# Performance work log

Measured on AMD Instinct MI355X. Metric: run time of the kernel, lower is better.

## Reference

```python
import jax, jax.numpy as jnp
import numpy as np

K = 20
EPS = 1e-5
SLOPE = 0.2

def knn(x, k):
    # x: [B, C, N]; returns indices of k nearest neighbors [B, N, k]
    xx = jnp.sum(x * x, axis=1)                      # [B, N]
    inner = jnp.einsum('bcn,bcm->bnm', x, x)         # [B, N, N]
    pd = -xx[:, :, None] + 2.0 * inner - xx[:, None, :]  # negative sq dist
    return jax.lax.top_k(pd, k)[1]

def leaky(y):
    return jnp.where(y > 0, y, SLOPE * y)

def batchnorm(y, g, b, axes):
    mean = jnp.mean(y, axis=axes, keepdims=True)
    var = jnp.var(y, axis=axes, keepdims=True)
    return (y - mean) / jnp.sqrt(var + EPS) * g + b

def edge_conv(x, W, g, b):
    # x: [B, C, N] -> [B, O, N]
    idx = knn(x, K)                                   # [B, N, k]
    xT = jnp.transpose(x, (0, 2, 1))                  # [B, N, C]
    nbr = jax.vmap(lambda xb, ib: xb[ib])(xT, idx)    # [B, N, k, C]
    ctr = jnp.broadcast_to(xT[:, :, None, :], nbr.shape)
    feat = jnp.concatenate([nbr - ctr, ctr], axis=-1) # [B, N, k, 2C]
    y = jnp.einsum('bnkc,oc->bnko', feat, W)          # 1x1 conv
    y = leaky(batchnorm(y, g, b, axes=(0, 1, 2)))
    return jnp.transpose(jnp.max(y, axis=2), (0, 2, 1))  # max over k -> [B, O, N]

def setup_inputs() -> dict:
    key = jax.random.key(0)
    ks = jax.random.split(key, 12)
    B, N = 8, 2048
    c1, c2, c3, c4, emb = 64, 64, 128, 256, 1024
    d = {
        'x':  jax.random.normal(ks[0], (B, 3, N), dtype=jnp.float32),
        'W1': jax.random.normal(ks[1], (c1, 6), dtype=jnp.float32) * 0.2,
        'W2': jax.random.normal(ks[2], (c2, 2 * c1), dtype=jnp.float32) * 0.1,
        'W3': jax.random.normal(ks[3], (c3, 2 * c2), dtype=jnp.float32) * 0.1,
        'W4': jax.random.normal(ks[4], (c4, 2 * c3), dtype=jnp.float32) * 0.08,
        'W5': jax.random.normal(ks[5], (emb, 2 * c4), dtype=jnp.float32) * 0.06,
        'g1': jnp.ones((c1,), jnp.float32), 'b1': jnp.zeros((c1,), jnp.float32),
        'g2': jnp.ones((c2,), jnp.float32), 'b2': jnp.zeros((c2,), jnp.float32),
        'g3': jnp.ones((c3,), jnp.float32), 'b3': jnp.zeros((c3,), jnp.float32),
        'g4': jnp.ones((c4,), jnp.float32), 'b4': jnp.zeros((c4,), jnp.float32),
        'g5': jnp.ones((emb,), jnp.float32), 'b5': jnp.zeros((emb,), jnp.float32),
    }
    return d

def reference(x, W1, W2, W3, W4, W5, g1, b1, g2, b2, g3, b3, g4, b4, g5, b5):
    x1 = edge_conv(x,  W1, g1, b1)   # [B, 64, N]
    x2 = edge_conv(x1, W2, g2, b2)   # [B, 64, N]
    x3 = edge_conv(x2, W3, g3, b3)   # [B, 128, N]
    x4 = edge_conv(x3, W4, g4, b4)   # [B, 256, N]
    cat = jnp.concatenate([x1, x2, x3, x4], axis=1)  # [B, 512, N]
    y = jnp.einsum('bcn,oc->bon', cat, W5)           # [B, 1024, N]
    y = leaky(batchnorm(y, g5[None, :, None], b5[None, :, None], axes=(0, 2)))
    mx = jnp.max(y, axis=2)
    av = jnp.mean(y, axis=2)
    return jnp.concatenate([mx, av], axis=1)         # [B, 2048]
```

## Files before the change

### kernel.cpp

```cpp
#include <hip/hip_runtime.h>
#include <cfloat>

#define BB 8
#define NN 2048
#define KNN 20
#define NCOPY 64
#define EPSV 1e-5f
#define SLOPEV 0.2f

typedef short bf16x8 __attribute__((ext_vector_type(8)));
typedef float f32x4 __attribute__((ext_vector_type(4)));

__device__ __forceinline__ unsigned short f2b(float f) {
    unsigned u = __builtin_bit_cast(unsigned, f);
    unsigned r = (u + 0x7FFFu + ((u >> 16) & 1u)) >> 16;
    return (unsigned short)r;
}
__device__ __forceinline__ short4 f2b4(float4 v) {
    short4 r;
    r.x = (short)f2b(v.x); r.y = (short)f2b(v.y);
    r.z = (short)f2b(v.z); r.w = (short)f2b(v.w);
    return r;
}
__device__ __forceinline__ bf16x8 f2b8(float4 a, float4 b) {
    short4 sa = f2b4(a), sb = f2b4(b);
    bf16x8 r;
    r[0] = sa.x; r[1] = sa.y; r[2] = sa.z; r[3] = sa.w;
    r[4] = sb.x; r[5] = sb.y; r[6] = sb.z; r[7] = sb.w;
    return r;
}


__global__ void transpose0_kernel(const float* __restrict__ x, float* __restrict__ XT0) {
    int e = blockIdx.x * blockDim.x + threadIdx.x;
    if (e >= BB * NN * 3) return;
    int b = e / (NN * 3); int r = e - b * NN * 3; int n = r / 3; int c = r - n * 3;
    XT0[e] = x[((size_t)b * 3 + c) * NN + n];
}

__global__ void wprep_kernel(const float* __restrict__ W, float* __restrict__ WaT,
                             float* __restrict__ WdT, int C, int O) {
    int e = blockIdx.x * blockDim.x + threadIdx.x;
    if (e >= C * O) return;
    int c = e / O, o = e - c * O;
    float a = W[o * 2 * C + c];
    WaT[e] = a;
    WdT[e] = W[o * 2 * C + C + c] - a;
}

__global__ void wprep4b_kernel(const float* __restrict__ W, short* __restrict__ Wab,
                               short* __restrict__ Wdb) {
    int e = blockIdx.x * 256 + threadIdx.x;
    int o = e >> 7, c = e & 127;
    float a = W[o * 256 + c];
    Wab[e] = (short)f2b(a);
    Wdb[e] = (short)f2b(W[o * 256 + 128 + c] - a);
}

__global__ void w5b_kernel(const float* __restrict__ W5, short* __restrict__ W5b) {
    int e = blockIdx.x * 256 + threadIdx.x;
    W5b[e] = (short)f2b(W5[e]);
}


template <int C>
__global__ void xx_kernel(const float* __restrict__ XT, float* __restrict__ xx) {
    int e = blockIdx.x * blockDim.x + threadIdx.x;
    if (e >= BB * NN) return;
    const float* p = &XT[(size_t)e * C];
    float s;
    if constexpr (C % 4 == 0) {
        float s0 = 0, s1 = 0, s2 = 0, s3 = 0;
        for (int c = 0; c < C; c += 4) {
            float4 v = *(const float4*)(p + c);
            s0 += v.x * v.x; s1 += v.y * v.y; s2 += v.z * v.z; s3 += v.w * v.w;
        }
        s = (s0 + s1) + (s2 + s3);
    } else {
        s = p[0] * p[0];
        for (int c = 1; c < C; ++c) s += p[c] * p[c];
    }
    xx[e] = s;
}


template <int C>
__global__ __launch_bounds__(256) void knn_dist_kernel(
    const float* __restrict__ XC,
    const float* __restrict__ XT,
    const float* __restrict__ xx,
    float* __restrict__ pd2,
    int b0) {
    constexpr int BK = 16;
    __shared__ float As[BK][68];
    __shared__ alignas(16) float Bs[BK][64];
    int mt = blockIdx.x, nt = blockIdx.y, bz = blockIdx.z;
    int b = b0 + bz;
    int n0 = nt * 64, m0 = mt * 64;
    int tid = threadIdx.x;
    int tn = tid >> 4, tm = tid & 15;
    float P[4][4][4];
    #pragma unroll
    for (int cl = 0; cl < 4; ++cl)
        #pragma unroll
        for (int i = 0; i < 4; ++i)
            #pragma unroll
            for (int j = 0; j < 4; ++j) P[cl][i][j] = 0.f;

    int arow = tid >> 2, acq = tid & 3;
    int brow = tid >> 4, bmq = tid & 15;
    for (int kb = 0; kb < C / BK; ++kb) {
        if (kb) __syncthreads();
        float4 av = *(const float4*)&XT[((size_t)b * NN + n0 + arow) * C + kb * BK + acq * 4];
        As[acq * 4 + 0][arow] = av.x; As[acq * 4 + 1][arow] = av.y;
        As[acq * 4 + 2][arow] = av.z; As[acq * 4 + 3][arow] = av.w;
        *(float4*)&Bs[brow][bmq * 4] =
            *(const float4*)&XC[((size_t)b * C + kb * BK + brow) * NN + m0 + bmq * 4];
        __syncthreads();
        #pragma unroll
        for (int c = 0; c < BK; ++c) {
            float4 a = *(const float4*)&As[c][tn * 4];
            float4 bv = *(const float4*)&Bs[c][tm * 4];
            int cl = c & 3;
            P[cl][0][0] += a.x * bv.x; P[cl][0][1] += a.x * bv.y; P[cl][0][2] += a.x * bv.z; P[cl][0][3] += a.x * bv.w;
            P[cl][1][0] += a.y * bv.x; P[cl][1][1] += a.y * bv.y; P[cl][1][2] += a.y * bv.z; P[cl][1][3] += a.y * bv.w;
            P[cl][2][0] += a.z * bv.x; P[cl][2][1] += a.z * bv.y; P[cl][2][2] += a.z * bv.z; P[cl][2][3] += a.z * bv.w;
            P[cl][3][0] += a.w * bv.x; P[cl][3][1] += a.w * bv.y; P[cl][3][2] += a.w * bv.z; P[cl][3][3] += a.w * bv.w;
        }
    }
    float4 xm = *(const float4*)&xx[(size_t)b * NN + m0 + tm * 4];
    #pragma unroll
    for (int i = 0; i < 4; ++i) {
        float xrn = xx[(size_t)b * NN + n0 + tn * 4 + i];
        float4 pd;
        float in0 = (P[0][i][0] + P[1][i][0]) + (P[2][i][0] + P[3][i][0]);
        float in1 = (P[0][i][1] + P[1][i][1]) + (P[2][i][1] + P[3][i][1]);
        float in2 = (P[0][i][2] + P[1][i][2]) + (P[2][i][2] + P[3][i][2]);
        float in3 = (P[0][i][3] + P[1][i][3]) + (P[2][i][3] + P[3][i][3]);
        pd.x = (2.0f * in0 - xrn) - xm.x;
        pd.y = (2.0f * in1 - xrn) - xm.y;
        pd.z = (2.0f * in2 - xrn) - xm.z;
        pd.w = (2.0f * in3 - xrn) - xm.w;
        *(float4*)&pd2[((size_t)bz * NN + n0 + tn * 4 + i) * NN + m0 + tm * 4] = pd;
    }
}

#define INS(val, mm) do { \
    float _v = (val); int _m = (mm); \
    bool b1 = _v > v1, b2 = _v > v2, b3 = _v > v3, b4 = _v > v4; \
    i4 = b3 ? i3 : (b4 ? _m : i4);  v4 = b3 ? v3 : (b4 ? _v : v4); \
    i3 = b2 ? i2 : (b3 ? _m : i3);  v3 = b2 ? v2 : (b3 ? _v : v3); \
    i2 = b1 ? i1 : (b2 ? _m : i2);  v2 = b1 ? v1 : (b2 ? _v : v2); \
    i1 = b1 ? _m : i1;              v1 = b1 ? _v : v1; \
} while (0)

__device__ __forceinline__ void sel20_reg(const float4* pv, int lane, int* outp) {
    float v1 = -FLT_MAX, v2 = -FLT_MAX, v3 = -FLT_MAX, v4 = -FLT_MAX;
    int i1 = 0x7FFFFFFF, i2 = 0x7FFFFFFF, i3 = 0x7FFFFFFF, i4 = 0x7FFFFFFF;
    unsigned rm = 0;
    #pragma unroll
    for (int j = 0; j < 8; ++j) {
        int m0 = 4 * lane + 256 * j;
        INS(pv[j].x, m0); INS(pv[j].y, m0 + 1); INS(pv[j].z, m0 + 2); INS(pv[j].w, m0 + 3);
    }
    int depth = 4;
    for (int it = 0; it < KNN; ++it) {
        float bv = v1;
        #pragma unroll
        for (int off = 1; off < 64; off <<= 1) bv = fmaxf(bv, __shfl_xor(bv, off));
        int cand = (v1 == bv) ? i1 : 0x7FFFFFFF;
        int bi = cand;
        #pragma unroll
        for (int off = 1; off < 64; off <<= 1) bi = min(bi, __shfl_xor(bi, off));
        if (lane == 0) outp[it] = bi;
        if (v1 == bv && i1 == bi) {
            rm |= 1u << ((((unsigned)bi >> 6) & 0x1C) | ((unsigned)bi & 3));
            v1 = v2; i1 = i2; v2 = v3; i2 = i3; v3 = v4; i3 = i4;
            v4 = -FLT_MAX; i4 = 0x7FFFFFFF;
            if (--depth == 0) {
                v1 = v2 = v3 = v4 = -FLT_MAX;
                i1 = i2 = i3 = i4 = 0x7FFFFFFF;
                #pragma unroll
                for (int j = 0; j < 8; ++j) {
                    int m0 = 4 * lane + 256 * j;
                    if (!(rm & (1u << (4 * j + 0)))) INS(pv[j].x, m0);
                    if (!(rm & (1u << (4 * j + 1)))) INS(pv[j].y, m0 + 1);
                    if (!(rm & (1u << (4 * j + 2)))) INS(pv[j].z, m0 + 2);
                    if (!(rm & (1u << (4 * j + 3)))) INS(pv[j].w, m0 + 3);
                }
                depth = 4;
            }
        }
    }
}

__global__ __launch_bounds__(256) void knn_sel_kernel(
    const float* __restrict__ pd2, int* __restrict__ idxb, int b0) {
    int tid = threadIdx.x, w = tid >> 6, lane = tid & 63;
    int rg = blockIdx.x * 4 + w;
    int bz = rg >> 11, n = rg & (NN - 1);
    const float* row = pd2 + ((size_t)bz * NN + n) * NN;
    float4 pv[8];
    #pragma unroll
    for (int j = 0; j < 8; ++j) pv[j] = *(const float4*)&row[4 * lane + 256 * j];
    int* outp = idxb + ((size_t)(b0 + bz) * NN + n) * KNN;
    sel20_reg(pv, lane, outp);
}

__global__ __launch_bounds__(256) void knn_c3_kernel(
    const float* __restrict__ XC,
    const float* __restrict__ XT,
    const float* __restrict__ xx, int* __restrict__ idxb) {
    int tid = threadIdx.x, w = tid >> 6, lane = tid & 63;
    int rg = blockIdx.x * 4 + w;
    int b = rg >> 11, n = rg & (NN - 1);
    const float* xt0 = XT + ((size_t)b * NN + n) * 3;
    float s0 = xt0[0], s1 = xt0[1], s2 = xt0[2];
    float xrn = xx[(size_t)b * NN + n];
    float4 pv[8];
    #pragma unroll
    for (int j = 0; j < 8; ++j) {
        int m0 = 4 * lane + 256 * j;
        float4 v0 = *(const float4*)&XC[((size_t)b * 3 + 0) * NN + m0];
        float4 v1 = *(const float4*)&XC[((size_t)b * 3 + 1) * NN + m0];
        float4 v2 = *(const float4*)&XC[((size_t)b * 3 + 2) * NN + m0];
        float4 xm = *(const float4*)&xx[(size_t)b * NN + m0];
        float4 in;
        in.x = v0.x * s0; in.x += v1.x * s1; in.x += v2.x * s2;
        in.y = v0.y * s0; in.y += v1.y * s1; in.y += v2.y * s2;
        in.z = v0.z * s0; in.z += v1.z * s1; in.z += v2.z * s2;
        in.w = v0.w * s0; in.w += v1.w * s1; in.w += v2.w * s2;
        pv[j].x = (2.0f * in.x - xrn) - xm.x;
        pv[j].y = (2.0f * in.y - xrn) - xm.y;
        pv[j].z = (2.0f * in.z - xrn) - xm.z;
        pv[j].w = (2.0f * in.w - xrn) - xm.w;
    }
    int* outp = idxb + ((size_t)b * NN + n) * KNN;
    sel20_reg(pv, lane, outp);
}
#undef INS


template <int C, int O>
__global__ __launch_bounds__(256) void edge_passA_kernel(
    const float* __restrict__ XT, const int* __restrict__ idxb,
    const float* __restrict__ WaT, const float* __restrict__ WdT,
    float* __restrict__ ymaxb, float* __restrict__ yminb, float* __restrict__ stats) {
    constexpr int OT = O / 4;
    constexpr int G = 256 / OT;
    constexpr int KP = (KNN + G - 1) / G;
    constexpr int CP = (C % 4 == 0) ? (C + 4) : C;
    __shared__ alignas(16) float ctr[C];
    __shared__ alignas(16) float nbr[KNN][CP];
    __shared__ alignas(16) float t2[O];
    __shared__ int sidx[KNN];
    __shared__ alignas(16) float red[4][1024];
    int blk = blockIdx.x;
    int b = blk >> 11;
    int tid = threadIdx.x;
    if (tid < KNN) sidx[tid] = idxb[(size_t)blk * KNN + tid];
    for (int e = tid; e < C; e += 256) ctr[e] = XT[(size_t)blk * C + e];
    __syncthreads();
    if constexpr (C % 4 == 0) {
        for (int e = tid; e < KNN * (C / 4); e += 256) {
            int k = e / (C / 4), q = e - k * (C / 4);
            *(float4*)&nbr[k][q * 4] =
                *(const float4*)&XT[((size_t)b * NN + sidx[k]) * C + q * 4];
        }
    } else {
        for (int e = tid; e < KNN * C; e += 256) {
            int k = e / C, c = e - k * C;
            nbr[k][c] = XT[((size_t)b * NN + sidx[k]) * C + c];
        }
    }
    if (tid < O) {
        float s = 0;
        for (int c = 0; c < C; ++c) s += WdT[c * O + tid] * ctr[c];
        t2[tid] = s;
    }
    __syncthreads();
    int og = tid % OT, kg = tid / OT;
    int o0 = og * 4;
    float acc[KP][4];
    #pragma unroll
    for (int j = 0; j < KP; ++j) { acc[j][0] = 0; acc[j][1] = 0; acc[j][2] = 0; acc[j][3] = 0; }
    if constexpr (C % 4 == 0) {
        for (int c = 0; c < C; c += 4) {
            float4 w0 = *(const float4*)&WaT[(c + 0) * O + o0];
            float4 w1 = *(const float4*)&WaT[(c + 1) * O + o0];
            float4 w2 = *(const float4*)&WaT[(c + 2) * O + o0];
            float4 w3 = *(const float4*)&WaT[(c + 3) * O + o0];
            #pragma unroll
            for (int j = 0; j < KP; ++j) {
                int k = kg + j * G;
                if (k < KNN) {
                    float4 nv = *(const float4*)&nbr[k][c];
                    acc[j][0] += nv.x * w0.x + nv.y * w1.x + nv.z * w2.x + nv.w * w3.x;
                    acc[j][1] += nv.x * w0.y + nv.y * w1.y + nv.z * w2.y + nv.w * w3.y;
                    acc[j][2] += nv.x * w0.z + nv.y * w1.z + nv.z * w2.z + nv.w * w3.z;
                    acc[j][3] += nv.x * w0.w + nv.y * w1.w + nv.z * w2.w + nv.w * w3.w;
                }
            }
        }
    } else {
        for (int c = 0; c < C; ++c) {
            float4 w = *(const float4*)&WaT[c * O + o0];
            #pragma unroll
            for (int j = 0; j < KP; ++j) {
                int k = kg + j * G;
                if (k < KNN) {
                    float nv = nbr[k][c];
                    acc[j][0] += nv * w.x; acc[j][1] += nv * w.y;
                    acc[j][2] += nv * w.z; acc[j][3] += nv * w.w;
                }
            }
        }
    }
    float t2a[4];
    *(float4*)t2a = *(const float4*)&t2[o0];
    float vmax[4], vmin[4], vsum[4], vsq[4];
    #pragma unroll
    for (int q = 0; q < 4; ++q) { vmax[q] = -FLT_MAX; vmin[q] = FLT_MAX; vsum[q] = 0; vsq[q] = 0; }
    #pragma unroll
    for (int j = 0; j < KP; ++j) {
        int k = kg + j * G;
        if (k < KNN) {
            #pragma unroll
            for (int q = 0; q < 4; ++q) {
                float y = acc[j][q] + t2a[q];
                vmax[q] = fmaxf(vmax[q], y); vmin[q] = fminf(vmin[q], y);
                vsum[q] += y; vsq[q] += y * y;
            }
        }
    }
    *(float4*)&red[0][kg * O + o0] = make_float4(vmax[0], vmax[1], vmax[2], vmax[3]);
    *(float4*)&red[1][kg * O + o0] = make_float4(vmin[0], vmin[1], vmin[2], vmin[3]);
    *(float4*)&red[2][kg * O + o0] = make_float4(vsum[0], vsum[1], vsum[2], vsum[3]);
    *(float4*)&red[3][kg * O + o0] = make_float4(vsq[0], vsq[1], vsq[2], vsq[3]);
    __syncthreads();
    if (tid < O) {
        float m1 = -FLT_MAX, m2 = FLT_MAX, s1 = 0, s2 = 0;
        #pragma unroll 4
        for (int g = 0; g < G; ++g) {
            m1 = fmaxf(m1, red[0][g * O + tid]);
            m2 = fminf(m2, red[1][g * O + tid]);
            s1 += red[2][g * O + tid];
            s2 += red[3][g * O + tid];
        }
        ymaxb[(size_t)blk * O + tid] = m1;
        yminb[(size_t)blk * O + tid] = m2;
        float* st = &stats[(size_t)(blk & (NCOPY - 1)) * (2 * O)];
        atomicAdd(&st[tid], s1);
        atomicAdd(&st[O + tid], s2);
    }
}


__global__ __launch_bounds__(256) void t2_mfma_kernel(
    const float* __restrict__ XT3, const short* __restrict__ Wdb, float* __restrict__ T2) {
    __shared__ alignas(16) short A[16][136];
    int blk = blockIdx.x;
    int tid = threadIdx.x, w = tid >> 6, lane = tid & 63;
    int n0g = blk * 16;
    for (int ch = tid; ch < 512; ch += 256) {
        int r = ch >> 5, c4 = (ch & 31) << 2;
        float4 v = *(const float4*)&XT3[((size_t)n0g + r) * 128 + c4];
        *(short4*)&A[r][c4] = f2b4(v);
    }
    __syncthreads();
    int arow = lane & 15, aq = lane >> 4;
    bf16x8 af[4];
    #pragma unroll
    for (int ks = 0; ks < 4; ++ks)
        af[ks] = *(const bf16x8*)&A[arow][ks * 32 + aq * 8];
    for (int t = 0; t < 4; ++t) {
        int nt = w * 4 + t;
        f32x4 acc = {0.f, 0.f, 0.f, 0.f};
        const short* bp = Wdb + (size_t)(nt * 16 + arow) * 128 + aq * 8;
        #pragma unroll
        for (int ks = 0; ks < 4; ++ks)
            acc = __builtin_amdgcn_mfma_f32_16x16x32_bf16(af[ks], *(const bf16x8*)(bp + ks * 32), acc, 0, 0, 0);
        #pragma unroll
        for (int r = 0; r < 4; ++r)
            T2[((size_t)n0g + aq * 4 + r) * 256 + nt * 16 + arow] = acc[r];
    }
}


__global__ __launch_bounds__(256) void edge4_mfma_kernel(
    const float* __restrict__ XT, const int* __restrict__ idxb,
    const short* __restrict__ Wab, const float* __restrict__ T2,
    float* __restrict__ ymaxb, float* __restrict__ yminb, float* __restrict__ stats) {
    int blk = blockIdx.x;
    int tid = threadIdx.x, w = tid >> 6, lane = tid & 63;
    int p = blk * 4 + w;
    int b = p >> 11;
    size_t baseC = (size_t)b * NN;
    const int* idxp = idxb + (size_t)p * KNN;
    int arow = lane & 15, aq = lane >> 4;
    int idx0 = idxp[arow];
    int idx1 = (arow < 4) ? idxp[16 + arow] : idx0;
    const float* r0 = &XT[(baseC + idx0) * 128 + aq * 8];
    const float* r1 = &XT[(baseC + idx1) * 128 + aq * 8];
    bf16x8 af0[4], af1[4];
    #pragma unroll
    for (int ks = 0; ks < 4; ++ks) {
        af0[ks] = f2b8(*(const float4*)(r0 + ks * 32), *(const float4*)(r0 + ks * 32 + 4));
        af1[ks] = f2b8(*(const float4*)(r1 + ks * 32), *(const float4*)(r1 + ks * 32 + 4));
    }
    const float* t2p = T2 + (size_t)p * 256;
    float* st = stats + (size_t)(p & (NCOPY - 1)) * 512;
    const short* bp0 = Wab + (size_t)arow * 128 + aq * 8;
    bf16x8 bfc[4];
    #pragma unroll
    for (int ks = 0; ks < 4; ++ks) bfc[ks] = *(const bf16x8*)(bp0 + ks * 32);
    float t2c = t2p[arow];
    for (int nt = 0; nt < 16; ++nt) {
        bf16x8 bfn[4]; float t2n = 0.f;
        if (nt < 15) {
            const short* bpn = Wab + (size_t)((nt + 1) * 16 + arow) * 128 + aq * 8;
            #pragma unroll
            for (int ks = 0; ks < 4; ++ks) bfn[ks] = *(const bf16x8*)(bpn + ks * 32);
            t2n = t2p[(nt + 1) * 16 + arow];
        }
        f32x4 acc0 = {0.f, 0.f, 0.f, 0.f}, acc1 = {0.f, 0.f, 0.f, 0.f};
        #pragma unroll
        for (int ks = 0; ks < 4; ++ks) {
            acc0 = __builtin_amdgcn_mfma_f32_16x16x32_bf16(af0[ks], bfc[ks], acc0, 0, 0, 0);
            acc1 = __builtin_amdgcn_mfma_f32_16x16x32_bf16(af1[ks], bfc[ks], acc1, 0, 0, 0);
        }
        float lmax = -FLT_MAX, lmin = FLT_MAX, ls = 0.f, lsq = 0.f;
        #pragma unroll
        for (int r = 0; r < 4; ++r) {
            float y = acc0[r] + t2c;
            lmax = fmaxf(lmax, y); lmin = fminf(lmin, y); ls += y; lsq += y * y;
        }
        if (aq == 0) {
            #pragma unroll
            for (int r = 0; r < 4; ++r) {
                float y = acc1[r] + t2c;
                lmax = fmaxf(lmax, y); lmin = fminf(lmin, y); ls += y; lsq += y * y;
            }
        }
        #pragma unroll
        for (int off = 16; off < 64; off <<= 1) {
            lmax = fmaxf(lmax, __shfl_xor(lmax, off));
            lmin = fminf(lmin, __shfl_xor(lmin, off));
            ls += __shfl_xor(ls, off);
            lsq += __shfl_xor(lsq, off);
        }
        if (lane < 16) {
            ymaxb[(size_t)p * 256 + nt * 16 + lane] = lmax;
            yminb[(size_t)p * 256 + nt * 16 + lane] = lmin;
            atomicAdd(&st[nt * 16 + lane], ls);
            atomicAdd(&st[256 + nt * 16 + lane], lsq);
        }
        #pragma unroll
        for (int ks = 0; ks < 4; ++ks) bfc[ks] = bfn[ks];
        t2c = t2n;
    }
}


__global__ void finalize_stats_kernel(const float* __restrict__ stats, const float* __restrict__ gg,
                                      const float* __restrict__ bb, float* __restrict__ scsh,
                                      int O, float invM) {
    int o = blockIdx.x * blockDim.x + threadIdx.x;
    if (o >= O) return;
    float s1 = 0, s2 = 0;
    for (int cp = 0; cp < NCOPY; ++cp) {
        s1 += stats[(size_t)cp * 2 * O + o];
        s2 += stats[(size_t)cp * 2 * O + O + o];
    }
    float mean = s1 * invM;
    float var = s2 * invM - mean * mean;
    float scale = gg[o] * rsqrtf(var + EPSV);
    float shift = bb[o] - mean * scale;
    scsh[o] = scale; scsh[O + o] = shift;
}

__global__ void edge_passB_kernel(const float* __restrict__ ymaxb, const float* __restrict__ yminb,
                                  const float* __restrict__ scsh, float* __restrict__ XTout,
                                  float* __restrict__ XCout, int O, int total) {
    int e = blockIdx.x * blockDim.x + threadIdx.x;
    if (e >= total) return;
    int o = e & (O - 1);
    float sc = scsh[o], sh = scsh[O + o];
    float y = (sc >= 0.0f) ? ymaxb[e] : yminb[e];
    float z = sc * y + sh;
    float r = (z > 0.0f) ? z : SLOPEV * z;
    XTout[e] = r;
    if (XCout) {
        int n = (e / O) & (NN - 1);
        int bb_ = e / (O * NN);
        XCout[((size_t)bb_ * O + o) * NN + n] = r;
    }
}


__device__ __forceinline__ void stage_cat_b(short (*A)[520], const float* __restrict__ XT1,
                                            const float* __restrict__ XT2, const float* __restrict__ XT3,
                                            const float* __restrict__ XT4, int n0g, int tid) {
    for (int ch = tid; ch < 32 * 16; ch += 256) { int r = ch >> 4, c4 = (ch & 15) << 2;
        *(short4*)&A[r][c4]       = f2b4(*(const float4*)&XT1[((size_t)n0g + r) * 64 + c4]); }
    for (int ch = tid; ch < 32 * 16; ch += 256) { int r = ch >> 4, c4 = (ch & 15) << 2;
        *(short4*)&A[r][64 + c4]  = f2b4(*(const float4*)&XT2[((size_t)n0g + r) * 64 + c4]); }
    for (int ch = tid; ch < 32 * 32; ch += 256) { int r = ch >> 5, c4 = (ch & 31) << 2;
        *(short4*)&A[r][128 + c4] = f2b4(*(const float4*)&XT3[((size_t)n0g + r) * 128 + c4]); }
    for (int ch = tid; ch < 32 * 64; ch += 256) { int r = ch >> 6, c4 = (ch & 63) << 2;
        *(short4*)&A[r][256 + c4] = f2b4(*(const float4*)&XT4[((size_t)n0g + r) * 256 + c4]); }
}

__global__ __launch_bounds__(256) void final_mfmaA_kernel(
    const float* __restrict__ XT1, const float* __restrict__ XT2, const float* __restrict__ XT3,
    const float* __restrict__ XT4, const short* __restrict__ W5b, float* __restrict__ stats) {
    __shared__ alignas(16) short A[32][520];
    int blk = blockIdx.x;
    int tid = threadIdx.x, w = tid >> 6, lane = tid & 63;
    int n0g = blk * 32;
    stage_cat_b(A, XT1, XT2, XT3, XT4, n0g, tid);
    __syncthreads();
    int arow = lane & 15, aq = lane >> 4;
    float* st = stats + (size_t)(blk & (NCOPY - 1)) * 2048;
    for (int mt = 0; mt < 2; ++mt) {
        bf16x8 af[16];
        #pragma unroll
        for (int ks = 0; ks < 16; ++ks)
            af[ks] = *(const bf16x8*)&A[mt * 16 + arow][ks * 32 + aq * 8];
        for (int t = 0; t < 16; ++t) {
            int nt = w * 16 + t;
            f32x4 acc = {0.f, 0.f, 0.f, 0.f};
            const short* bp = W5b + (size_t)(nt * 16 + arow) * 512 + aq * 8;
            #pragma unroll
            for (int ks = 0; ks < 16; ++ks)
                acc = __builtin_amdgcn_mfma_f32_16x16x32_bf16(af[ks], *(const bf16x8*)(bp + ks * 32), acc, 0, 0, 0);
            float ls = (acc[0] + acc[1]) + (acc[2] + acc[3]);
            float lsq = (acc[0] * acc[0] + acc[1] * acc[1]) + (acc[2] * acc[2] + acc[3] * acc[3]);
            ls += __shfl_xor(ls, 16); ls += __shfl_xor(ls, 32);
            lsq += __shfl_xor(lsq, 16); lsq += __shfl_xor(lsq, 32);
            if (lane < 16) {
                atomicAdd(&st[nt * 16 + lane], ls);
                atomicAdd(&st[1024 + nt * 16 + lane], lsq);
            }
        }
    }
}

__global__ __launch_bounds__(256) void final_mfmaB_kernel(
    const float* __restrict__ XT1, const float* __restrict__ XT2, const float* __restrict__ XT3,
    const float* __restrict__ XT4, const short* __restrict__ W5b, const float* __restrict__ scsh,
    float* __restrict__ pmax, float* __restrict__ psum) {
    __shared__ alignas(16) short A[32][520];
    int blk = blockIdx.x;
    int tid = threadIdx.x, w = tid >> 6, lane = tid & 63;
    int n0g = blk * 32;
    stage_cat_b(A, XT1, XT2, XT3, XT4, n0g, tid);
    __syncthreads();
    int arow = lane & 15, aq = lane >> 4;
    for (int mt = 0; mt < 2; ++mt) {
        bf16x8 af[16];
        #pragma unroll
        for (int ks = 0; ks < 16; ++ks)
            af[ks] = *(const bf16x8*)&A[mt * 16 + arow][ks * 32 + aq * 8];
        for (int t = 0; t < 16; ++t) {
            int nt = w * 16 + t;
            f32x4 acc = {0.f, 0.f, 0.f, 0.f};
            const short* bp = W5b + (size_t)(nt * 16 + arow) * 512 + aq * 8;
            #pragma unroll
            for (int ks = 0; ks < 16; ++ks)
                acc = __builtin_amdgcn_mfma_f32_16x16x32_bf16(af[ks], *(const bf16x8*)(bp + ks * 32), acc, 0, 0, 0);
            int o = nt * 16 + arow;
            float sc = scsh[o], sh = scsh[1024 + o];
            float lmax = -FLT_MAX, lsm = 0.f;
            #pragma unroll
            for (int r = 0; r < 4; ++r) {
                float z = fmaf(sc, acc[r], sh);
                float l = (z > 0.0f) ? z : SLOPEV * z;
                lmax = fmaxf(lmax, l); lsm += l;
            }
            lmax = fmaxf(lmax, __shfl_xor(lmax, 16));
            lmax = fmaxf(lmax, __shfl_xor(lmax, 32));
            lsm += __shfl_xor(lsm, 16); lsm += __shfl_xor(lsm, 32);
            if (lane < 16) {
                pmax[(size_t)(blk * 2 + mt) * 1024 + o] = lmax;
                psum[(size_t)(blk * 2 + mt) * 1024 + o] = lsm;
            }
        }
    }
}

__global__ void final_passC_kernel(const float* __restrict__ pmax, const float* __restrict__ psum,
                                   float* __restrict__ out) {
    int e = blockIdx.x * blockDim.x + threadIdx.x;
    if (e >= BB * 1024) return;
    int b = e >> 10, o = e & 1023;
    float mx = -FLT_MAX, sm = 0;
    for (int j = 0; j < NN / 16; ++j) {
        size_t p = ((size_t)(b * (NN / 16) + j)) * 1024 + o;
        mx = fmaxf(mx, pmax[p]);
        sm += psum[p];
    }
    out[b * 2048 + o] = mx;
    out[b * 2048 + 1024 + o] = sm * (1.0f / NN);
}


extern "C" void kernel_launch(void* const* d_in, const int* in_sizes, int n_in,
                              void* d_out, int out_size, void* d_ws, size_t ws_size,
                              hipStream_t stream) {
    const float* x  = (const float*)d_in[0];
    const float* W1 = (const float*)d_in[1];
    const float* W2 = (const float*)d_in[2];
    const float* W3 = (const float*)d_in[3];
    const float* W4 = (const float*)d_in[4];
    const float* W5 = (const float*)d_in[5];
    const float* g1 = (const float*)d_in[6];  const float* b1 = (const float*)d_in[7];
    const float* g2 = (const float*)d_in[8];  const float* b2 = (const float*)d_in[9];
    const float* g3 = (const float*)d_in[10]; const float* b3 = (const float*)d_in[11];
    const float* g4 = (const float*)d_in[12]; const float* b4 = (const float*)d_in[13];
    const float* g5 = (const float*)d_in[14]; const float* b5 = (const float*)d_in[15];

    float* ws = (float*)d_ws;
    size_t off = 0;
    float* XT0 = ws + off; off += (size_t)BB * NN * 3;
    float* XT1 = ws + off; off += (size_t)BB * NN * 64;
    float* XT2 = ws + off; off += (size_t)BB * NN * 64;
    float* XT3 = ws + off; off += (size_t)BB * NN * 128;
    float* XT4 = ws + off; off += (size_t)BB * NN * 256;
    float* XC1 = ws + off; off += (size_t)BB * NN * 64;
    float* XC2 = ws + off; off += (size_t)BB * NN * 64;
    float* XC3 = ws + off; off += (size_t)BB * NN * 128;
    float* ymax = ws + off; off += (size_t)BB * NN * 256;
    float* ymin = ws + off; off += (size_t)BB * NN * 256;
    int*   idxb = (int*)(ws + off); off += (size_t)BB * NN * KNN;
    float* xxb = ws + off; off += (size_t)BB * NN;
    float* WaT = ws + off; off += 128 * 256;
    float* WdT = ws + off; off += 128 * 256;
    short* Wa4b = (short*)(ws + off); off += 256 * 128 / 2;
    short* Wd4b = (short*)(ws + off); off += 256 * 128 / 2;
    short* W5b  = (short*)(ws + off); off += 1024 * 512 / 2;
    float* st1 = ws + off; off += NCOPY * 2 * 64;
    float* st2 = ws + off; off += NCOPY * 2 * 64;
    float* st3 = ws + off; off += NCOPY * 2 * 128;
    float* st4 = ws + off; off += NCOPY * 2 * 256;
    float* st5 = ws + off; off += NCOPY * 2 * 1024;
    float* sc1 = ws + off; off += 2 * 64;
    float* sc2 = ws + off; off += 2 * 64;
    float* sc3 = ws + off; off += 2 * 128;
    float* sc4 = ws + off; off += 2 * 256;
    float* sc5 = ws + off; off += 2 * 1024;
    float* T2 = XC1;
    float* pd2 = ymax;
    float* pmax = ymax;
    float* psum = ymin;

    hipMemsetAsync(st1, 0, (size_t)NCOPY * 2 * (64 + 64 + 128 + 256 + 1024) * sizeof(float), stream);

    transpose0_kernel<<<(BB * NN * 3 + 255) / 256, 256, 0, stream>>>(x, XT0);

    dim3 dgrid(NN / 64, NN / 64, 2);

    wprep_kernel<<<(3 * 64 + 255) / 256, 256, 0, stream>>>(W1, WaT, WdT, 3, 64);
    xx_kernel<3><<<BB * NN / 256, 256, 0, stream>>>(XT0, xxb);
    knn_c3_kernel<<<BB * NN / 4, 256, 0, stream>>>(x, XT0, xxb, idxb);
    edge_passA_kernel<3, 64><<<BB * NN, 256, 0, stream>>>(XT0, idxb, WaT, WdT, ymax, ymin, st1);
    finalize_stats_kernel<<<1, 64, 0, stream>>>(st1, g1, b1, sc1, 64, 1.0f / ((float)BB * NN * KNN));
    edge_passB_kernel<<<BB * NN * 64 / 256, 256, 0, stream>>>(ymax, ymin, sc1, XT1, XC1, 64, BB * NN * 64);

    wprep_kernel<<<(64 * 64 + 255) / 256, 256, 0, stream>>>(W2, WaT, WdT, 64, 64);
    xx_kernel<64><<<BB * NN / 256, 256, 0, stream>>>(XT1, xxb);
    for (int p = 0; p < 4; ++p) {
        knn_dist_kernel<64><<<dgrid, 256, 0, stream>>>(XC1, XT1, xxb, pd2, 2 * p);
        knn_sel_kernel<<<2 * NN / 4, 256, 0, stream>>>(pd2, idxb, 2 * p);
    }
    edge_passA_kernel<64, 64><<<BB * NN, 256, 0, stream>>>(XT1, idxb, WaT, WdT, ymax, ymin, st2);
    finalize_stats_kernel<<<1, 64, 0, stream>>>(st2, g2, b2, sc2, 64, 1.0f / ((float)BB * NN * KNN));
    edge_passB_kernel<<<BB * NN * 64 / 256, 256, 0, stream>>>(ymax, ymin, sc2, XT2, XC2, 64, BB * NN * 64);

    wprep_kernel<<<(64 * 128 + 255) / 256, 256, 0, stream>>>(W3, WaT, WdT, 64, 128);
    xx_kernel<64><<<BB * NN / 256, 256, 0, stream>>>(XT2, xxb);
    for (int p = 0; p < 4; ++p) {
        knn_dist_kernel<64><<<dgrid, 256, 0, stream>>>(XC2, XT2, xxb, pd2, 2 * p);
        knn_sel_kernel<<<2 * NN / 4, 256, 0, stream>>>(pd2, idxb, 2 * p);
    }
    edge_passA_kernel<64, 128><<<BB * NN, 256, 0, stream>>>(XT2, idxb, WaT, WdT, ymax, ymin, st3);
    finalize_stats_kernel<<<1, 128, 0, stream>>>(st3, g3, b3, sc3, 128, 1.0f / ((float)BB * NN * KNN));
    edge_passB_kernel<<<BB * NN * 128 / 256, 256, 0, stream>>>(ymax, ymin, sc3, XT3, XC3, 128, BB * NN * 128);

    wprep4b_kernel<<<256 * 128 / 256, 256, 0, stream>>>(W4, Wa4b, Wd4b);
    xx_kernel<128><<<BB * NN / 256, 256, 0, stream>>>(XT3, xxb);
    for (int p = 0; p < 4; ++p) {
        knn_dist_kernel<128><<<dgrid, 256, 0, stream>>>(XC3, XT3, xxb, pd2, 2 * p);
        knn_sel_kernel<<<2 * NN / 4, 256, 0, stream>>>(pd2, idxb, 2 * p);
    }
    t2_mfma_kernel<<<BB * NN / 16, 256, 0, stream>>>(XT3, Wd4b, T2);
    edge4_mfma_kernel<<<BB * NN / 4, 256, 0, stream>>>(XT3, idxb, Wa4b, T2, ymax, ymin, st4);
    finalize_stats_kernel<<<1, 256, 0, stream>>>(st4, g4, b4, sc4, 256, 1.0f / ((float)BB * NN * KNN));
    edge_passB_kernel<<<BB * NN * 256 / 256, 256, 0, stream>>>(ymax, ymin, sc4, XT4, nullptr, 256, BB * NN * 256);

    w5b_kernel<<<1024 * 512 / 256, 256, 0, stream>>>(W5, W5b);
    final_mfmaA_kernel<<<BB * NN / 32, 256, 0, stream>>>(XT1, XT2, XT3, XT4, W5b, st5);
    finalize_stats_kernel<<<4, 256, 0, stream>>>(st5, g5, b5, sc5, 1024, 1.0f / ((float)BB * NN));
    final_mfmaB_kernel<<<BB * NN / 32, 256, 0, stream>>>(XT1, XT2, XT3, XT4, W5b, sc5, pmax, psum);
    final_passC_kernel<<<(BB * 1024 + 255) / 256, 256, 0, stream>>>(pmax, psum, (float*)d_out);

    (void)in_sizes; (void)n_in; (void)out_size; (void)ws_size;
}
```

Baseline: 1.516 ms.

## Precompute per-point W·x projections and gather them instead of recomputing per neighbor

The edge-conv GEMM is factored as W_a·x_j + W_d·x_i, so T1 and T2 are computed once per point. A gather-reduce kernel then forms max/min/sum/sumsq over the k neighbors, which cuts the GEMM work by a factor of k. Atomic stat accumulation into NCOPY slots and the memset are replaced by per-block partial sums that finalize_stats reduces. Layer 4 now reuses the bf16 MFMA kernel to produce T1. The cost is extra global traffic for the T1/T2 buffers, which alias existing workspace.

Result: faster. 1.400 ms (-7.6%).

```diff
diff --git a/kernel.cpp b/kernel.cpp
--- a/kernel.cpp
+++ b/kernel.cpp
@@ -4,7 +4,6 @@
 #define BB 8
 #define NN 2048
 #define KNN 20
-#define NCOPY 64
 #define EPSV 1e-5f
 #define SLOPEV 0.2f
 
@@ -20,13 +19,6 @@
     short4 r;
     r.x = (short)f2b(v.x); r.y = (short)f2b(v.y);
     r.z = (short)f2b(v.z); r.w = (short)f2b(v.w);
-    return r;
-}
-__device__ __forceinline__ bf16x8 f2b8(float4 a, float4 b) {
-    short4 sa = f2b4(a), sb = f2b4(b);
-    bf16x8 r;
-    r[0] = sa.x; r[1] = sa.y; r[2] = sa.z; r[3] = sa.w;
-    r[4] = sb.x; r[5] = sb.y; r[6] = sb.z; r[7] = sb.w;
     return r;
 }
 
@@ -242,116 +234,136 @@
 
 
 template <int C, int O>
-__global__ __launch_bounds__(256) void edge_passA_kernel(
-    const float* __restrict__ XT, const int* __restrict__ idxb,
-    const float* __restrict__ WaT, const float* __restrict__ WdT,
-    float* __restrict__ ymaxb, float* __restrict__ yminb, float* __restrict__ stats) {
-    constexpr int OT = O / 4;
-    constexpr int G = 256 / OT;
-    constexpr int KP = (KNN + G - 1) / G;
-    constexpr int CP = (C % 4 == 0) ? (C + 4) : C;
-    __shared__ alignas(16) float ctr[C];
-    __shared__ alignas(16) float nbr[KNN][CP];
-    __shared__ alignas(16) float t2[O];
-    __shared__ int sidx[KNN];
-    __shared__ alignas(16) float red[4][1024];
-    int blk = blockIdx.x;
-    int b = blk >> 11;
+__global__ __launch_bounds__(256) void t1t2_gemm_kernel(
+    const float* __restrict__ XT, const float* __restrict__ WaT,
+    const float* __restrict__ WdT, float* __restrict__ T1, float* __restrict__ T2) {
+    constexpr int CP = (C < 4) ? 4 : C;
+    __shared__ alignas(16) float xt[64][CP];
+    int p0 = blockIdx.x * 64;
     int tid = threadIdx.x;
-    if (tid < KNN) sidx[tid] = idxb[(size_t)blk * KNN + tid];
-    for (int e = tid; e < C; e += 256) ctr[e] = XT[(size_t)blk * C + e];
+    if constexpr (C % 4 == 0) {
+        for (int e = tid; e < 64 * (C / 4); e += 256) {
+            int r = e / (C / 4), q = e - r * (C / 4);
+            *(float4*)&xt[r][q * 4] = *(const float4*)&XT[((size_t)p0 + r) * C + q * 4];
+        }
+    } else {
+        for (int e = tid; e < 64 * C; e += 256) {
+            int r = e / C, c = e - r * C;
+            xt[r][c] = XT[((size_t)p0 + r) * C + c];
+        }
+    }
     __syncthreads();
-    if constexpr (C % 4 == 0) {
-        for (int e = tid; e < KNN * (C / 4); e += 256) {
-            int k = e / (C / 4), q = e - k * (C / 4);
-            *(float4*)&nbr[k][q * 4] =
-                *(const float4*)&XT[((size_t)b * NN + sidx[k]) * C + q * 4];
-        }
-    } else {
-        for (int e = tid; e < KNN * C; e += 256) {
-            int k = e / C, c = e - k * C;
-            nbr[k][c] = XT[((size_t)b * NN + sidx[k]) * C + c];
-        }
-    }
-    if (tid < O) {
-        float s = 0;
-        for (int c = 0; c < C; ++c) s += WdT[c * O + tid] * ctr[c];
-        t2[tid] = s;
-    }
-    __syncthreads();
-    int og = tid % OT, kg = tid / OT;
-    int o0 = og * 4;
-    float acc[KP][4];
-    #pragma unroll
-    for (int j = 0; j < KP; ++j) { acc[j][0] = 0; acc[j][1] = 0; acc[j][2] = 0; acc[j][3] = 0; }
-    if constexpr (C % 4 == 0) {
-        for (int c = 0; c < C; c += 4) {
-            float4 w0 = *(const float4*)&WaT[(c + 0) * O + o0];
-            float4 w1 = *(const float4*)&WaT[(c + 1) * O + o0];
-            float4 w2 = *(const float4*)&WaT[(c + 2) * O + o0];
-            float4 w3 = *(const float4*)&WaT[(c + 3) * O + o0];
-            #pragma unroll
-            for (int j = 0; j < KP; ++j) {
-                int k = kg + j * G;
-                if (k < KNN) {
-                    float4 nv = *(const float4*)&nbr[k][c];
-                    acc[j][0] += nv.x * w0.x + nv.y * w1.x + nv.z * w2.x + nv.w * w3.x;
-                    acc[j][1] += nv.x * w0.y + nv.y * w1.y + nv.z * w2.y + nv.w * w3.y;
-                    acc[j][2] += nv.x * w0.z + nv.y * w1.z + nv.z * w2.z + nv.w * w3.z;
-                    acc[j][3] += nv.x * w0.w + nv.y * w1.w + nv.z * w2.w + nv.w * w3.w;
+    {
+        constexpr int OQ = O / 4;
+        constexpr int PS = 256 / OQ;
+        constexpr int PPT = 64 / PS;
+        int oq = tid % OQ, ps = tid / OQ;
+        int o0 = oq * 4;
+        float acc[PPT][4];
+        #pragma unroll
+        for (int t = 0; t < PPT; ++t) { acc[t][0] = 0; acc[t][1] = 0; acc[t][2] = 0; acc[t][3] = 0; }
+        if constexpr (C % 4 == 0) {
+            for (int c = 0; c < C; c += 4) {
+                float4 w0 = *(const float4*)&WaT[(c + 0) * O + o0];
+                float4 w1 = *(const float4*)&WaT[(c + 1) * O + o0];
+                float4 w2 = *(const float4*)&WaT[(c + 2) * O + o0];
+                float4 w3 = *(const float4*)&WaT[(c + 3) * O + o0];
+                #pragma unroll
+                for (int t = 0; t < PPT; ++t) {
+                    float4 nv = *(const float4*)&xt[ps + t * PS][c];
+                    acc[t][0] += nv.x * w0.x + nv.y * w1.x + nv.z * w2.x + nv.w * w3.x;
+                    acc[t][1] += nv.x * w0.y + nv.y * w1.y + nv.z * w2.y + nv.w * w3.y;
+                    acc[t][2] += nv.x * w0.z + nv.y * w1.z + nv.z * w2.z + nv.w * w3.z;
+                    acc[t][3] += nv.x * w0.w + nv.y * w1.w + nv.z * w2.w + nv.w * w3.w;
                 }
             }
-        }
-    } else {
-        for (int c = 0; c < C; ++c) {
-            float4 w = *(const float4*)&WaT[c * O + o0];
-            #pragma unroll
-            for (int j = 0; j < KP; ++j) {
-                int k = kg + j * G;
-                if (k < KNN) {
-                    float nv = nbr[k][c];
-                    acc[j][0] += nv * w.x; acc[j][1] += nv * w.y;
-                    acc[j][2] += nv * w.z; acc[j][3] += nv * w.w;
+        } else {
+            for (int c = 0; c < C; ++c) {
+                float4 w = *(const float4*)&WaT[c * O + o0];
+                #pragma unroll
+                for (int t = 0; t < PPT; ++t) {
+                    float nv = xt[ps + t * PS][c];
+                    acc[t][0] += nv * w.x; acc[t][1] += nv * w.y;
+                    acc[t][2] += nv * w.z; acc[t][3] += nv * w.w;
                 }
             }
         }
-    }
-    float t2a[4];
-    *(float4*)t2a = *(const float4*)&t2[o0];
-    float vmax[4], vmin[4], vsum[4], vsq[4];
-    #pragma unroll
-    for (int q = 0; q < 4; ++q) { vmax[q] = -FLT_MAX; vmin[q] = FLT_MAX; vsum[q] = 0; vsq[q] = 0; }
-    #pragma unroll
-    for (int j = 0; j < KP; ++j) {
-        int k = kg + j * G;
-        if (k < KNN) {
+        #pragma unroll
+        for (int t = 0; t < PPT; ++t)
+            *(float4*)&T1[((size_t)p0 + ps + t * PS) * O + o0] =
+                make_float4(acc[t][0], acc[t][1], acc[t][2], acc[t][3]);
+    }
+    {
+        constexpr int PS2 = 256 / O;
+        constexpr int PPT2 = 64 / PS2;
+        int o = tid % O, ps = tid / O;
+        float s[PPT2];
+        #pragma unroll
+        for (int t = 0; t < PPT2; ++t) s[t] = 0.f;
+        for (int c = 0; c < C; ++c) {
+            float w = WdT[c * O + o];
             #pragma unroll
-            for (int q = 0; q < 4; ++q) {
-                float y = acc[j][q] + t2a[q];
-                vmax[q] = fmaxf(vmax[q], y); vmin[q] = fminf(vmin[q], y);
-                vsum[q] += y; vsq[q] += y * y;
-            }
-        }
-    }
-    *(float4*)&red[0][kg * O + o0] = make_float4(vmax[0], vmax[1], vmax[2], vmax[3]);
-    *(float4*)&red[1][kg * O + o0] = make_float4(vmin[0], vmin[1], vmin[2], vmin[3]);
-    *(float4*)&red[2][kg * O + o0] = make_float4(vsum[0], vsum[1], vsum[2], vsum[3]);
-    *(float4*)&red[3][kg * O + o0] = make_float4(vsq[0], vsq[1], vsq[2], vsq[3]);
+            for (int t = 0; t < PPT2; ++t) s[t] += w * xt[ps + t * PS2][c];
+        }
+        #pragma unroll
+        for (int t = 0; t < PPT2; ++t) T2[((size_t)p0 + ps + t * PS2) * O + o] = s[t];
+    }
+}
+
+
+template <int O, int G>
+__global__ __launch_bounds__(256) void edge_reduce_kernel(
+    const float* __restrict__ T1, const float* __restrict__ T2,
+    const int* __restrict__ idxb,
+    float* __restrict__ ymaxb, float* __restrict__ yminb, float* __restrict__ stP) {
+    constexpr int OQ = O / 4;
+    constexpr int PTS = 256 / OQ;
+    __shared__ int sidx[PTS][KNN];
+    __shared__ alignas(16) float red[2][PTS][O];
+    int blk = blockIdx.x, tid = threadIdx.x;
+    int oq = tid % OQ, ps = tid / OQ;
+    int o0 = oq * 4;
+    float4 as = make_float4(0, 0, 0, 0), aq = make_float4(0, 0, 0, 0);
+    for (int g = 0; g < G; ++g) {
+        int pbase = (blk * G + g) * PTS;
+        if (g) __syncthreads();
+        for (int e = tid; e < PTS * KNN; e += 256)
+            sidx[e / KNN][e % KNN] = idxb[(size_t)(pbase + e / KNN) * KNN + (e % KNN)];
+        __syncthreads();
+        int p = pbase + ps;
+        int b = p >> 11;
+        float4 t2v = *(const float4*)&T2[(size_t)p * O + o0];
+        float4 vmax = make_float4(-FLT_MAX, -FLT_MAX, -FLT_MAX, -FLT_MAX);
+        float4 vmin = make_float4(FLT_MAX, FLT_MAX, FLT_MAX, FLT_MAX);
+        float4 vs = make_float4(0, 0, 0, 0), vq = make_float4(0, 0, 0, 0);
+        #pragma unroll 4
+        for (int k = 0; k < KNN; ++k) {
+            int r = (b << 11) + sidx[ps][k];
+            float4 t1v = *(const float4*)&T1[(size_t)r * O + o0];
+            float yx = t1v.x + t2v.x, yy = t1v.y + t2v.y;
+            float yz = t1v.z + t2v.z, yw = t1v.w + t2v.w;
+            vmax.x = fmaxf(vmax.x, yx); vmax.y = fmaxf(vmax.y, yy);
+            vmax.z = fmaxf(vmax.z, yz); vmax.w = fmaxf(vmax.w, yw);
+            vmin.x = fminf(vmin.x, yx); vmin.y = fminf(vmin.y, yy);
+            vmin.z = fminf(vmin.z, yz); vmin.w = fminf(vmin.w, yw);
+            vs.x += yx; vs.y += yy; vs.z += yz; vs.w += yw;
+            vq.x += yx * yx; vq.y += yy * yy; vq.z += yz * yz; vq.w += yw * yw;
+        }
+        *(float4*)&ymaxb[(size_t)p * O + o0] = vmax;
+        *(float4*)&yminb[(size_t)p * O + o0] = vmin;
+        as.x += vs.x; as.y += vs.y; as.z += vs.z; as.w += vs.w;
+        aq.x += vq.x; aq.y += vq.y; aq.z += vq.z; aq.w += vq.w;
+    }
     __syncthreads();
-    if (tid < O) {
-        float m1 = -FLT_MAX, m2 = FLT_MAX, s1 = 0, s2 = 0;
+    *(float4*)&red[0][ps][o0] = as;
+    *(float4*)&red[1][ps][o0] = aq;
+    __syncthreads();
+    for (int e = tid; e < 2 * O; e += 256) {
+        int pl = e / O, oo = e - pl * O;
+        float s = red[pl][0][oo];
         #pragma unroll 4
-        for (int g = 0; g < G; ++g) {
-            m1 = fmaxf(m1, red[0][g * O + tid]);
-            m2 = fminf(m2, red[1][g * O + tid]);
-            s1 += red[2][g * O + tid];
-            s2 += red[3][g * O + tid];
-        }
-        ymaxb[(size_t)blk * O + tid] = m1;
-        yminb[(size_t)blk * O + tid] = m2;
-        float* st = &stats[(size_t)(blk & (NCOPY - 1)) * (2 * O)];
-        atomicAdd(&st[tid], s1);
-        atomicAdd(&st[O + tid], s2);
+        for (int j = 1; j < PTS; ++j) s += red[pl][j][oo];
+        stP[(size_t)blk * 2 * O + e] = s;
     }
 }
 
@@ -387,91 +399,26 @@
 }
 
 
-__global__ __launch_bounds__(256) void edge4_mfma_kernel(
-    const float* __restrict__ XT, const int* __restrict__ idxb,
-    const short* __restrict__ Wab, const float* __restrict__ T2,
-    float* __restrict__ ymaxb, float* __restrict__ yminb, float* __restrict__ stats) {
-    int blk = blockIdx.x;
-    int tid = threadIdx.x, w = tid >> 6, lane = tid & 63;
-    int p = blk * 4 + w;
-    int b = p >> 11;
-    size_t baseC = (size_t)b * NN;
-    const int* idxp = idxb + (size_t)p * KNN;
-    int arow = lane & 15, aq = lane >> 4;
-    int idx0 = idxp[arow];
-    int idx1 = (arow < 4) ? idxp[16 + arow] : idx0;
-    const float* r0 = &XT[(baseC + idx0) * 128 + aq * 8];
-    const float* r1 = &XT[(baseC + idx1) * 128 + aq * 8];
-    bf16x8 af0[4], af1[4];
-    #pragma unroll
-    for (int ks = 0; ks < 4; ++ks) {
-        af0[ks] = f2b8(*(const float4*)(r0 + ks * 32), *(const float4*)(r0 + ks * 32 + 4));
-        af1[ks] = f2b8(*(const float4*)(r1 + ks * 32), *(const float4*)(r1 + ks * 32 + 4));
-    }
-    const float* t2p = T2 + (size_t)p * 256;
-    float* st = stats + (size_t)(p & (NCOPY - 1)) * 512;
-    const short* bp0 = Wab + (size_t)arow * 128 + aq * 8;
-    bf16x8 bfc[4];
-    #pragma unroll
-    for (int ks = 0; ks < 4; ++ks) bfc[ks] = *(const bf16x8*)(bp0 + ks * 32);
-    float t2c = t2p[arow];
-    for (int nt = 0; nt < 16; ++nt) {
-        bf16x8 bfn[4]; float t2n = 0.f;
-        if (nt < 15) {
-            const short* bpn = Wab + (size_t)((nt + 1) * 16 + arow) * 128 + aq * 8;
-            #pragma unroll
-            for (int ks = 0; ks < 4; ++ks) bfn[ks] = *(const bf16x8*)(bpn + ks * 32);
-            t2n = t2p[(nt + 1) * 16 + arow];
-        }
-        f32x4 acc0 = {0.f, 0.f, 0.f, 0.f}, acc1 = {0.f, 0.f, 0.f, 0.f};
-        #pragma unroll
-        for (int ks = 0; ks < 4; ++ks) {
-            acc0 = __builtin_amdgcn_mfma_f32_16x16x32_bf16(af0[ks], bfc[ks], acc0, 0, 0, 0);
-            acc1 = __builtin_amdgcn_mfma_f32_16x16x32_bf16(af1[ks], bfc[ks], acc1, 0, 0, 0);
-        }
-        float lmax = -FLT_MAX, lmin = FLT_MAX, ls = 0.f, lsq = 0.f;
-        #pragma unroll
-        for (int r = 0; r < 4; ++r) {
-            float y = acc0[r] + t2c;
-            lmax = fmaxf(lmax, y); lmin = fminf(lmin, y); ls += y; lsq += y * y;
-        }
-        if (aq == 0) {
-            #pragma unroll
-            for (int r = 0; r < 4; ++r) {
-                float y = acc1[r] + t2c;
-                lmax = fmaxf(lmax, y); lmin = fminf(lmin, y); ls += y; lsq += y * y;
-            }
-        }
-        #pragma unroll
-        for (int off = 16; off < 64; off <<= 1) {
-            lmax = fmaxf(lmax, __shfl_xor(lmax, off));
-            lmin = fminf(lmin, __shfl_xor(lmin, off));
-            ls += __shfl_xor(ls, off);
-            lsq += __shfl_xor(lsq, off);
-        }
-        if (lane < 16) {
-            ymaxb[(size_t)p * 256 + nt * 16 + lane] = lmax;
-            yminb[(size_t)p * 256 + nt * 16 + lane] = lmin;
-            atomicAdd(&st[nt * 16 + lane], ls);
-            atomicAdd(&st[256 + nt * 16 + lane], lsq);
-        }
-        #pragma unroll
-        for (int ks = 0; ks < 4; ++ks) bfc[ks] = bfn[ks];
-        t2c = t2n;
-    }
-}
-
-
-__global__ void finalize_stats_kernel(const float* __restrict__ stats, const float* __restrict__ gg,
+__global__ void finalize_stats_kernel(const float* __restrict__ stP, const float* __restrict__ gg,
                                       const float* __restrict__ bb, float* __restrict__ scsh,
-                                      int O, float invM) {
+                                      int O, int nblk, float invM) {
     int o = blockIdx.x * blockDim.x + threadIdx.x;
     if (o >= O) return;
-    float s1 = 0, s2 = 0;
-    for (int cp = 0; cp < NCOPY; ++cp) {
-        s1 += stats[(size_t)cp * 2 * O + o];
-        s2 += stats[(size_t)cp * 2 * O + O + o];
-    }
+    float sa[8] = {0, 0, 0, 0, 0, 0, 0, 0}, qa[8] = {0, 0, 0, 0, 0, 0, 0, 0};
+    int cp = 0;
+    for (; cp + 8 <= nblk; cp += 8) {
+        #pragma unroll
+        for (int j = 0; j < 8; ++j) {
+            sa[j] += stP[(size_t)(cp + j) * 2 * O + o];
+            qa[j] += stP[(size_t)(cp + j) * 2 * O + O + o];
+        }
+    }
+    for (; cp < nblk; ++cp) {
+        sa[0] += stP[(size_t)cp * 2 * O + o];
+        qa[0] += stP[(size_t)cp * 2 * O + O + o];
+    }
+    float s1 = ((sa[0] + sa[1]) + (sa[2] + sa[3])) + ((sa[4] + sa[5]) + (sa[6] + sa[7]));
+    float s2 = ((qa[0] + qa[1]) + (qa[2] + qa[3])) + ((qa[4] + qa[5]) + (qa[6] + qa[7]));
     float mean = s1 * invM;
     float var = s2 * invM - mean * mean;
     float scale = gg[o] * rsqrtf(var + EPSV);
@@ -513,7 +460,7 @@
 
 __global__ __launch_bounds__(256) void final_mfmaA_kernel(
     const float* __restrict__ XT1, const float* __restrict__ XT2, const float* __restrict__ XT3,
-    const float* __restrict__ XT4, const short* __restrict__ W5b, float* __restrict__ stats) {
+    const float* __restrict__ XT4, const short* __restrict__ W5b, float* __restrict__ stP5) {
     __shared__ alignas(16) short A[32][520];
     int blk = blockIdx.x;
     int tid = threadIdx.x, w = tid >> 6, lane = tid & 63;
@@ -521,7 +468,7 @@
     stage_cat_b(A, XT1, XT2, XT3, XT4, n0g, tid);
     __syncthreads();
     int arow = lane & 15, aq = lane >> 4;
-    float* st = stats + (size_t)(blk & (NCOPY - 1)) * 2048;
+    float* bp5 = stP5 + (size_t)blk * 2048;
     for (int mt = 0; mt < 2; ++mt) {
         bf16x8 af[16];
         #pragma unroll
@@ -539,8 +486,9 @@
             ls += __shfl_xor(ls, 16); ls += __shfl_xor(ls, 32);
             lsq += __shfl_xor(lsq, 16); lsq += __shfl_xor(lsq, 32);
             if (lane < 16) {
-                atomicAdd(&st[nt * 16 + lane], ls);
-                atomicAdd(&st[1024 + nt * 16 + lane], lsq);
+                int o = nt * 16 + lane;
+                if (mt == 0) { bp5[o] = ls; bp5[1024 + o] = lsq; }
+                else         { bp5[o] += ls; bp5[1024 + o] += lsq; }
             }
         }
     }
@@ -639,22 +587,20 @@
     short* Wa4b = (short*)(ws + off); off += 256 * 128 / 2;
     short* Wd4b = (short*)(ws + off); off += 256 * 128 / 2;
     short* W5b  = (short*)(ws + off); off += 1024 * 512 / 2;
-    float* st1 = ws + off; off += NCOPY * 2 * 64;
-    float* st2 = ws + off; off += NCOPY * 2 * 64;
-    float* st3 = ws + off; off += NCOPY * 2 * 128;
-    float* st4 = ws + off; off += NCOPY * 2 * 256;
-    float* st5 = ws + off; off += NCOPY * 2 * 1024;
+    float* stP = ws + off; off += 2048 * 256;
     float* sc1 = ws + off; off += 2 * 64;
     float* sc2 = ws + off; off += 2 * 64;
     float* sc3 = ws + off; off += 2 * 128;
     float* sc4 = ws + off; off += 2 * 256;
     float* sc5 = ws + off; off += 2 * 1024;
-    float* T2 = XC1;
+    float* T1f = XT4;
+    float* T2f = XT4 + (size_t)BB * NN * 128;
+    float* T1_4 = XT4;
+    float* T2_4 = XC1;
     float* pd2 = ymax;
+    float* stP5 = ymax;
     float* pmax = ymax;
     float* psum = ymin;
-
-    hipMemsetAsync(st1, 0, (size_t)NCOPY * 2 * (64 + 64 + 128 + 256 + 1024) * sizeof(float), stream);
 
     transpose0_kernel<<<(BB * NN * 3 + 255) / 256, 256, 0, stream>>>(x, XT0);
 
@@ -663,8 +609,9 @@
     wprep_kernel<<<(3 * 64 + 255) / 256, 256, 0, stream>>>(W1, WaT, WdT, 3, 64);
     xx_kernel<3><<<BB * NN / 256, 256, 0, stream>>>(XT0, xxb);
     knn_c3_kernel<<<BB * NN / 4, 256, 0, stream>>>(x, XT0, xxb, idxb);
-    edge_passA_kernel<3, 64><<<BB * NN, 256, 0, stream>>>(XT0, idxb, WaT, WdT, ymax, ymin, st1);
-    finalize_stats_kernel<<<1, 64, 0, stream>>>(st1, g1, b1, sc1, 64, 1.0f / ((float)BB * NN * KNN));
+    t1t2_gemm_kernel<3, 64><<<BB * NN / 64, 256, 0, stream>>>(XT0, WaT, WdT, T1f, T2f);
+    edge_reduce_kernel<64, 1><<<BB * NN / 16, 256, 0, stream>>>(T1f, T2f, idxb, ymax, ymin, stP);
+    finalize_stats_kernel<<<1, 64, 0, stream>>>(stP, g1, b1, sc1, 64, BB * NN / 16, 1.0f / ((float)BB * NN * KNN));
     edge_passB_kernel<<<BB * NN * 64 / 256, 256, 0, stream>>>(ymax, ymin, sc1, XT1, XC1, 64, BB * NN * 64);
 
     wprep_kernel<<<(64 * 64 + 255) / 256, 256, 0, stream>>>(W2, WaT, WdT, 64, 64);
@@ -673,8 +620,9 @@
         knn_dist_kernel<64><<<dgrid, 256, 0, stream>>>(XC1, XT1, xxb, pd2, 2 * p);
         knn_sel_kernel<<<2 * NN / 4, 256, 0, stream>>>(pd2, idxb, 2 * p);
     }
-    edge_passA_kernel<64, 64><<<BB * NN, 256, 0, stream>>>(XT1, idxb, WaT, WdT, ymax, ymin, st2);
-    finalize_stats_kernel<<<1, 64, 0, stream>>>(st2, g2, b2, sc2, 64, 1.0f / ((float)BB * NN * KNN));
+    t1t2_gemm_kernel<64, 64><<<BB * NN / 64, 256, 0, stream>>>(XT1, WaT, WdT, T1f, T2f);
+    edge_reduce_kernel<64, 1><<<BB * NN / 16, 256, 0, stream>>>(T1f, T2f, idxb, ymax, ymin, stP);
+    finalize_stats_kernel<<<1, 64, 0, stream>>>(stP, g2, b2, sc2, 64, BB * NN / 16, 1.0f / ((float)BB * NN * KNN));
     edge_passB_kernel<<<BB * NN * 64 / 256, 256, 0, stream>>>(ymax, ymin, sc2, XT2, XC2, 64, BB * NN * 64);
 
     wprep_kernel<<<(64 * 128 + 255) / 256, 256, 0, stream>>>(W3, WaT, WdT, 64, 128);
@@ -683,8 +631,9 @@
         knn_dist_kernel<64><<<dgrid, 256, 0, stream>>>(XC2, XT2, xxb, pd2, 2 * p);
         knn_sel_kernel<<<2 * NN / 4, 256, 0, stream>>>(pd2, idxb, 2 * p);
     }
-    edge_passA_kernel<64, 128><<<BB * NN, 256, 0, stream>>>(XT2, idxb, WaT, WdT, ymax, ymin, st3);
-    finalize_stats_kernel<<<1, 128, 0, stream>>>(st3, g3, b3, sc3, 128, 1.0f / ((float)BB * NN * KNN));
+    t1t2_gemm_kernel<64, 128><<<BB * NN / 64, 256, 0, stream>>>(XT2, WaT, WdT, T1f, T2f);
+    edge_reduce_kernel<128, 1><<<BB * NN / 8, 256, 0, stream>>>(T1f, T2f, idxb, ymax, ymin, stP);
+    finalize_stats_kernel<<<1, 128, 0, stream>>>(stP, g3, b3, sc3, 128, BB * NN / 8, 1.0f / ((float)BB * NN * KNN));
     edge_passB_kernel<<<BB * NN * 128 / 256, 256, 0, stream>>>(ymax, ymin, sc3, XT3, XC3, 128, BB * NN * 128);
 
     wprep4b_kernel<<<256 * 128 / 256, 256, 0, stream>>>(W4, Wa4b, Wd4b);
@@ -693,14 +642,15 @@
         knn_dist_kernel<128><<<dgrid, 256, 0, stream>>>(XC3, XT3, xxb, pd2, 2 * p);
         knn_sel_kernel<<<2 * NN / 4, 256, 0, stream>>>(pd2, idxb, 2 * p);
     }
-    t2_mfma_kernel<<<BB * NN / 16, 256, 0, stream>>>(XT3, Wd4b, T2);
-    edge4_mfma_kernel<<<BB * NN / 4, 256, 0, stream>>>(XT3, idxb, Wa4b, T2, ymax, ymin, st4);
-    finalize_stats_kernel<<<1, 256, 0, stream>>>(st4, g4, b4, sc4, 256, 1.0f / ((float)BB * NN * KNN));
+    t2_mfma_kernel<<<BB * NN / 16, 256, 0, stream>>>(XT3, Wd4b, T2_4);
+    t2_mfma_kernel<<<BB * NN / 16, 256, 0, stream>>>(XT3, Wa4b, T1_4);
+    edge_reduce_kernel<256, 4><<<BB * NN / 16, 256, 0, stream>>>(T1_4, T2_4, idxb, ymax, ymin, stP);
+    finalize_stats_kernel<<<1, 256, 0, stream>>>(stP, g4, b4, sc4, 256, BB * NN / 16, 1.0f / ((float)BB * NN * KNN));
     edge_passB_kernel<<<BB * NN * 256 / 256, 256, 0, stream>>>(ymax, ymin, sc4, XT4, nullptr, 256, BB * NN * 256);
 
     w5b_kernel<<<1024 * 512 / 256, 256, 0, stream>>>(W5, W5b);
-    final_mfmaA_kernel<<<BB * NN / 32, 256, 0, stream>>>(XT1, XT2, XT3, XT4, W5b, st5);
-    finalize_stats_kernel<<<4, 256, 0, stream>>>(st5, g5, b5, sc5, 1024, 1.0f / ((float)BB * NN));
+    final_mfmaA_kernel<<<BB * NN / 32, 256, 0, stream>>>(XT1, XT2, XT3, XT4, W5b, stP5);
+    finalize_stats_kernel<<<4, 256, 0, stream>>>(stP5, g5, b5, sc5, 1024, BB * NN / 32, 1.0f / ((float)BB * NN));
     final_mfmaB_kernel<<<BB * NN / 32, 256, 0, stream>>>(XT1, XT2, XT3, XT4, W5b, sc5, pmax, psum);
     final_passC_kernel<<<(BB * 1024 + 255) / 256, 256, 0, stream>>>(pmax, psum, (float*)d_out);
 
```
